# Kernel optimization log

Measured on AMD Instinct MI355X. Metric: run time of the kernel, lower is better.

Reference implementation:

```python
import jax, jax.numpy as jnp
import numpy as np

EPS = 1e-5

def conv2d(x, w, pad):
    # x: NCHW, w: OIHW
    return jax.lax.conv_general_dilated(
        x, w, window_strides=(1, 1), padding=[(pad, pad), (pad, pad)],
        dimension_numbers=("NCHW", "OIHW", "NCHW"))

def instnorm(x, gamma=None, beta=None):
    # per-(N,C) normalization over H,W (biased variance, like torch InstanceNorm2d)
    mu = jnp.mean(x, axis=(2, 3), keepdims=True)
    var = jnp.mean((x - mu) ** 2, axis=(2, 3), keepdims=True)
    y = (x - mu) * jax.lax.rsqrt(var + EPS)
    if gamma is not None:
        y = y * gamma[None, :, None, None] + beta[None, :, None, None]
    return y

def ode_rhs(y, W, b):
    # conv -> relu -> instance norm (no affine) -> conv_transpose(same weight) -> -1 (stable)
    z = conv2d(y, W, 1) + b[None, :, None, None]
    z = jax.nn.relu(z)
    z = instnorm(z)
    # ConvTranspose2d with weight W (in,out,kh,kw here square C,C) == conv with
    # channel-swapped, spatially flipped kernel, SAME padding.
    Wt = jnp.transpose(jnp.flip(W, axis=(2, 3)), (1, 0, 2, 3))
    z = conv2d(z, Wt, 1)
    return -z

def ode_block(y, Wbank, bbank):
    # RK4 over t_grid = linspace(0,1,5): 4 steps of dt = 0.25.
    # Piecewise-constant weights: floor(t*4) clamped -> stages 1-3 of step i use
    # bank[i]; stage 4 (at t_{i+1}) uses bank[min(i+1, 3)].
    n = Wbank.shape[0]
    dt = 1.0 / n
    for i in range(n):
        j = min(i + 1, n - 1)
        k1 = ode_rhs(y, Wbank[i], bbank[i])
        k2 = ode_rhs(y + 0.5 * dt * k1, Wbank[i], bbank[i])
        k3 = ode_rhs(y + 0.5 * dt * k2, Wbank[i], bbank[i])
        k4 = ode_rhs(y + dt * k3, Wbank[j], bbank[j])
        y = y + (dt / 6.0) * (k1 + 2.0 * k2 + 2.0 * k3 + k4)
    return y

def avgpool2(x):
    N, C, H, W = x.shape
    return x.reshape(N, C, H // 2, 2, W // 2, 2).mean(axis=(3, 5))

def forward(x, stem_w, stem_b, norm1_g, norm1_b, ode1_W, ode1_b,
            conn1_w, conn1_b, norm3_g, norm3_b, ode2_W, ode2_b,
            conn2_w, conn2_b, norm4_g, norm4_b, ode3_W, ode3_b,
            head_w, head_b):
    x = conv2d(x, stem_w, 1) + stem_b[None, :, None, None]
    x = instnorm(x, norm1_g, norm1_b)
    x = jax.nn.relu(x)
    x = ode_block(x, ode1_W, ode1_b)
    x = conv2d(x, conn1_w, 0) + conn1_b[None, :, None, None]
    x = instnorm(x, norm3_g, norm3_b)
    x = jax.nn.relu(x)
    x = avgpool2(x)
    x = ode_block(x, ode2_W, ode2_b)
    x = conv2d(x, conn2_w, 0) + conn2_b[None, :, None, None]
    x = instnorm(x, norm4_g, norm4_b)
    x = jax.nn.relu(x)
    x = avgpool2(x)
    x = ode_block(x, ode3_W, ode3_b)
    x = x.mean(axis=(2, 3))  # AdaptiveAvgPool2d(1) + Flatten -> [N, 4*ch]
    return x @ head_w.T + head_b

def setup_inputs() -> dict:
    key = jax.random.key(0)
    ks = jax.random.split(key, 16)
    ch = 64
    f = jnp.float32
    d = {
        "x": jax.random.normal(ks[0], (8, 3, 96, 96), f),
        "stem_w": jax.random.normal(ks[1], (ch, 3, 3, 3), f) * 0.1,
        "stem_b": jnp.zeros((ch,), f),
        "norm1_g": jnp.ones((ch,), f),
        "norm1_b": jnp.zeros((ch,), f),
        "ode1_W": jax.random.normal(ks[2], (4, ch, ch, 3, 3), f) * 0.1,
        "ode1_b": jnp.zeros((4, ch), f),
        "conn1_w": jax.random.normal(ks[3], (2 * ch, ch, 1, 1), f) * 0.1,
        "conn1_b": jnp.zeros((2 * ch,), f),
        "norm3_g": jnp.ones((2 * ch,), f),
        "norm3_b": jnp.zeros((2 * ch,), f),
        "ode2_W": jax.random.normal(ks[4], (4, 2 * ch, 2 * ch, 3, 3), f) * 0.1,
        "ode2_b": jnp.zeros((4, 2 * ch), f),
        "conn2_w": jax.random.normal(ks[5], (4 * ch, 2 * ch, 1, 1), f) * 0.1,
        "conn2_b": jnp.zeros((4 * ch,), f),
        "norm4_g": jnp.ones((4 * ch,), f),
        "norm4_b": jnp.zeros((4 * ch,), f),
        "ode3_W": jax.random.normal(ks[6], (4, 4 * ch, 4 * ch, 3, 3), f) * 0.1,
        "ode3_b": jnp.zeros((4, 4 * ch), f),
        "head_w": jax.random.normal(ks[7], (10, 4 * ch), f) * 0.05,
        "head_b": jnp.zeros((10,), f),
    }
    return d

def reference(x, stem_w, stem_b, norm1_g, norm1_b, ode1_W, ode1_b,
              conn1_w, conn1_b, norm3_g, norm3_b, ode2_W, ode2_b,
              conn2_w, conn2_b, norm4_g, norm4_b, ode3_W, ode3_b,
              head_w, head_b):
    return forward(x, stem_w, stem_b, norm1_g, norm1_b, ode1_W, ode1_b,
                   conn1_w, conn1_b, norm3_g, norm3_b, ode2_W, ode2_b,
                   conn2_w, conn2_b, norm4_g, norm4_b, ode3_W, ode3_b,
                   head_w, head_b)
```

## Files before the change

### kernel.cpp

```cpp
#include <hip/hip_runtime.h>


typedef __attribute__((ext_vector_type(8)))  short  s16x8;
typedef __attribute__((ext_vector_type(16))) float  f32x16;

__device__ __forceinline__ unsigned short bf16_rtne(float f) {
    unsigned u = __builtin_bit_cast(unsigned, f);
    unsigned r = u + 0x7FFFu + ((u >> 16) & 1u);
    return (unsigned short)(r >> 16);
}
__device__ __forceinline__ void split2(float v, unsigned& h, unsigned& l) {
    unsigned u = __builtin_bit_cast(unsigned, v);
    h = (u + 0x7fffu + ((u >> 16) & 1u)) >> 16;
    float r = v - __builtin_bit_cast(float, h << 16);
    unsigned ur = __builtin_bit_cast(unsigned, r);
    l = (ur + 0x7fffu + ((ur >> 16) & 1u)) >> 16;
}
__device__ __forceinline__ unsigned packsplit(float v) {
    unsigned h, l; split2(v, h, l); return h | (l << 16);
}

__global__ __launch_bounds__(256) void pack_weights(
    const float* __restrict__ Wb, unsigned short* __restrict__ out, int C)
{
    const int dir = blockIdx.y;
    const int MT = C >> 5, ICC = C >> 4;
    const size_t TOT = (size_t)36 * C * C;
    size_t t = (size_t)blockIdx.x * 256 + threadIdx.x;
    if (t >= TOT) return;
    int j = t & 7;
    int l = (t >> 3) & 63;
    size_t r = t >> 9;
    int kp  = r % 9;  r /= 9;
    int mt  = r % MT; r /= MT;
    int icc = r % ICC; r /= ICC;
    int bank = (int)r;
    int oc = mt * 32 + (l & 31);
    int ic = icc * 16 + (l >> 5) * 8 + j;
    int kh = kp / 3, kw = kp % 3;
    float v;
    if (dir == 0)
        v = Wb[(((size_t)(bank * C + oc) * C + ic) * 3 + kh) * 3 + kw];
    else
        v = Wb[(((size_t)(bank * C + ic) * C + oc) * 3 + (2 - kh)) * 3 + (2 - kw)];
    unsigned short h = bf16_rtne(v);
    float hf = __builtin_bit_cast(float, (unsigned)h << 16);
    unsigned short lo = bf16_rtne(v - hf);
    size_t idx = ((((size_t)bank * ICC + icc) * MT + mt) * 9 + kp) * 1024 + l * 8 + j;
    unsigned short* base = out + (size_t)dir * 72 * C * C;
    base[idx] = h;
    base[idx + 512] = lo;
}

template<int NW, int MODE>
__global__ __launch_bounds__(NW * 64) void conv_mfma4(
    const void* __restrict__ in,
    const unsigned short* __restrict__ pA,
    const float* __restrict__ bias,
    const float* __restrict__ partI,
    float* __restrict__ partO,
    const float* __restrict__ ybase, float* __restrict__ accb,
    float* __restrict__ ydstF, unsigned* __restrict__ ydstS,
    int C, int H, int W, int tilesX, int tilesT, float inv_hw,
    int mode, float acoef, float dt6)
{
    constexpr bool CONV2 = (MODE == 2);
    constexpr int TPX = 16, TPY = 2 * NW;
    constexpr int HX = TPX + 2, HY = TPY + 2;
    constexpr int NROW = HX * HY;
    constexpr int RS = 20;
    constexpr int PL = NROW * RS;
    constexpr int BUFS = 2 * PL;
    constexpr int NTHR = NW * 64;
    constexpr int NELEM = NROW * 16;
    constexpr int NIT = (NELEM + NTHR - 1) / NTHR;
    __shared__ __align__(16) unsigned short sB[2 * BUFS];
    __shared__ float sTab[CONV2 ? 512 : 4];

    const int tid = threadIdx.x;
    const int w = tid >> 6, lane = tid & 63;
    const int n = blockIdx.x;
    const int tile = blockIdx.y;
    const int mt = blockIdx.z;
    const int tileX = tile % tilesX, tileY = tile / tilesX;
    const int px0 = tileX * TPX, py0 = tileY * TPY;
    const int ocb = mt * 32;
    const int HW = H * W;
    const int ICC = C >> 4, MT = C >> 5;
    const int col = lane & 31, half = lane >> 5;
    const int xl = col & 15, yr = col >> 4;
    const int wy0 = 2 * w;
    const int ncbase = n * C;

    float stg[NIT];
    auto stageLoad = [&](int icc) {
#pragma unroll
        for (int i = 0; i < NIT; i++) {
            int e = tid + i * NTHR;
            float v = 0.f;
            if (e < NELEM) {
                int ic = e / NROW; int r = e - ic * NROW;
                int yy = r / HX, xx = r - yy * HX;
                int gy = py0 + yy - 1, gx = px0 + xx - 1;
                if (gy >= 0 && gy < H && gx >= 0 && gx < W) {
                    int c = icc * 16 + ic;
                    size_t ad = (size_t)(ncbase + c) * HW + gy * W + gx;
                    if (MODE == 0)
                        v = ((const float*)in)[ad];
                    else
                        v = __builtin_bit_cast(float, ((const unsigned*)in)[ad]);
                }
            }
            stg[i] = v;
        }
    };
    auto stageWrite = [&](int b, int c0) {
#pragma unroll
        for (int i = 0; i < NIT; i++) {
            int e = tid + i * NTHR;
            if (e < NELEM) {
                int ic = e / NROW; int r = e - ic * NROW;
                unsigned h, l;
                if (MODE == 1) {
                    unsigned u = __builtin_bit_cast(unsigned, stg[i]);
                    h = u & 0xffffu; l = u >> 16;
                } else if (MODE == 2) {
                    int yy = r / HX, xx = r - yy * HX;
                    int gy = py0 + yy - 1, gx = px0 + xx - 1;
                    float v = 0.f;
                    if (gy >= 0 && gy < H && gx >= 0 && gx < W) {
                        unsigned u = __builtin_bit_cast(unsigned, stg[i]);
                        float vh = __builtin_bit_cast(float, u << 16);
                        float vl = __builtin_bit_cast(float, u & 0xffff0000u);
                        int c = c0 + ic;
                        v = (vh + vl - sTab[2 * c]) * sTab[2 * c + 1];
                    }
                    split2(v, h, l);
                } else {
                    split2(stg[i], h, l);
                }
                int off = b * BUFS + r * RS + ic;
                sB[off] = (unsigned short)h;
                sB[off + PL] = (unsigned short)l;
            }
        }
    };
    auto loadB = [&](int b, int kp, s16x8& oh, s16x8& ol) {
        int kh = kp / 3, kw = kp - kh * 3;
        int px = (wy0 + yr + kh) * HX + (xl + kw);
        int off = b * BUFS + px * RS + half * 8;
        oh = *(const s16x8*)&sB[off];
        ol = *(const s16x8*)&sB[off + PL];
    };

    f32x16 accA{}, accB{}, accC{};

    stageLoad(0);

    if (CONV2) {
        for (int c0 = tid; c0 < C; c0 += NTHR) {
            int mtc = c0 >> 5, occ = c0 & 31;
            const float* pb = partI + ((size_t)(n * MT + mtc) * tilesT) * 64 + occ;
            float s = 0.f, q = 0.f;
#pragma unroll 4
            for (int tt = 0; tt < tilesT; ++tt) {
                s += pb[(size_t)tt * 64];
                q += pb[(size_t)tt * 64 + 32];
            }
            float m = s * inv_hw;
            sTab[2 * c0] = m;
            sTab[2 * c0 + 1] = rsqrtf(fmaf(-m, m, q * inv_hw) + 1e-5f);
        }
        __syncthreads();
    }

    stageWrite(0, 0);
    __syncthreads();

    for (int icc = 0; icc < ICC; ++icc) {
        s16x8 aH[9], aL[9];
        {
            const unsigned short* ab =
                pA + ((size_t)(icc * MT + mt)) * 9216 + lane * 8;
#pragma unroll
            for (int kp = 0; kp < 9; ++kp) {
                aH[kp] = *(const s16x8*)(ab + kp * 1024);
                aL[kp] = *(const s16x8*)(ab + kp * 1024 + 512);
            }
        }
        const int b = icc & 1;
        if (icc + 1 < ICC) stageLoad(icc + 1);

        s16x8 bh, bl;
        loadB(b, 0, bh, bl);
#pragma unroll
        for (int kp = 0; kp < 9; ++kp) {
            s16x8 bhn, bln;
            if (kp < 8) loadB(b, kp + 1, bhn, bln);
            accA = __builtin_amdgcn_mfma_f32_32x32x16_bf16(aH[kp], bh, accA, 0, 0, 0);
            accB = __builtin_amdgcn_mfma_f32_32x32x16_bf16(aL[kp], bh, accB, 0, 0, 0);
            accC = __builtin_amdgcn_mfma_f32_32x32x16_bf16(aH[kp], bl, accC, 0, 0, 0);
            if (kp < 8) { bh = bhn; bl = bln; }
        }
        if (icc + 1 < ICC) {
            stageWrite(b ^ 1, (icc + 1) * 16);
            __syncthreads();
        }
    }

    const int gx = px0 + xl;
    const int gy = py0 + wy0 + yr;
    const bool valid = (gx < W);
    float* sred = (float*)sB;
#pragma unroll
    for (int r = 0; r < 16; r++) {
        int row = (r & 3) + 8 * (r >> 2) + 4 * half;
        int oc = ocb + row;
        size_t idx = (size_t)(ncbase + oc) * HW + (size_t)gy * W + gx;
        float v = accA[r] + accB[r] + accC[r];
        if (!CONV2) {
            v += bias[oc];
            v = fmaxf(v, 0.f);
            if (valid) ydstS[idx] = packsplit(v);
            float s = valid ? v : 0.f;
            float sq = s * s;
#pragma unroll
            for (int m = 1; m < 32; m <<= 1) {
                s  += __shfl_xor(s, m, 64);
                sq += __shfl_xor(sq, m, 64);
            }
            if ((lane & 31) == 0) {
                int slot = ((w * 2 + half) * 16 + r) * 2;
                sred[slot] = s;
                sred[slot + 1] = sq;
            }
        } else if (valid) {
            float k = -v;
            if (mode == 0) {
                accb[idx] = k;
                ydstS[idx] = packsplit(ybase[idx] + acoef * k);
            } else if (mode == 3) {
                ydstF[idx] = ybase[idx] + dt6 * (accb[idx] + k);
            } else {
                accb[idx] += 2.f * k;
                ydstS[idx] = packsplit(ybase[idx] + acoef * k);
            }
        }
    }
    if (!CONV2) {
        __syncthreads();
        if (tid < 32) {
            int h2 = (tid >> 2) & 1;
            int r  = (tid & 3) | ((tid >> 3) << 2);
            float s = 0.f, sq = 0.f;
#pragma unroll
            for (int wv = 0; wv < NW; wv++) {
                int slot = ((wv * 2 + h2) * 16 + r) * 2;
                s  += sred[slot];
                sq += sred[slot + 1];
            }
            float* po = partO + ((size_t)(n * MT + mt) * tilesT + tile) * 64;
            po[tid] = s;
            po[tid + 32] = sq;
        }
    }
}

__global__ __launch_bounds__(256) void conv3x3_stem(
    const float* __restrict__ in, const float* __restrict__ w,
    const float* __restrict__ bias, float* __restrict__ out,
    int H, int W, int tilesX)
{
    __shared__ float sIn[3][18][34];
    __shared__ float sW[16][3][9];
    const int tid = threadIdx.x;
    const int tx = tid & 15, ty = tid >> 4;
    const int tileX = blockIdx.x % tilesX, tileY = blockIdx.x / tilesX;
    const int x0 = tileX * 32, y0 = tileY * 16;
    const int oc0 = blockIdx.y * 16;
    const int n = blockIdx.z;
    const int HW = H * W;

    for (int idx = tid; idx < 3 * 18 * 34; idx += 256) {
        int c = idx / (18 * 34); int r = idx % (18 * 34);
        int iy = r / 34, ix = r % 34;
        int gy = y0 + iy - 1, gx = x0 + ix - 1;
        float v = 0.f;
        if (gy >= 0 && gy < H && gx >= 0 && gx < W)
            v = in[(size_t)(n * 3 + c) * HW + gy * W + gx];
        sIn[c][iy][ix] = v;
    }
    for (int idx = tid; idx < 16 * 27; idx += 256) {
        int o = idx / 27, r = idx % 27;
        sW[o][r / 9][r % 9] = w[(size_t)(oc0 + o) * 27 + r];
    }
    __syncthreads();

    float a0[16], a1[16];
#pragma unroll
    for (int o = 0; o < 16; o++) { a0[o] = 0.f; a1[o] = 0.f; }
#pragma unroll
    for (int c = 0; c < 3; c++)
#pragma unroll
        for (int kh = 0; kh < 3; kh++)
#pragma unroll
            for (int kw = 0; kw < 3; kw++) {
                float v0 = sIn[c][ty + kh][tx + kw];
                float v1 = sIn[c][ty + kh][tx + 16 + kw];
#pragma unroll
                for (int o = 0; o < 16; o++) {
                    float wv = sW[o][c][kh * 3 + kw];
                    a0[o] = fmaf(v0, wv, a0[o]);
                    a1[o] = fmaf(v1, wv, a1[o]);
                }
            }

    const int gy = y0 + ty, gx = x0 + tx;
#pragma unroll
    for (int o = 0; o < 16; o++) {
        float bb = bias[oc0 + o];
        size_t base = (size_t)(n * 64 + oc0 + o) * HW + (size_t)gy * W + gx;
        out[base] = a0[o] + bb;
        out[base + 16] = a1[o] + bb;
    }
}

__global__ __launch_bounds__(256) void stats_kernel(
    const float* __restrict__ x, float* __restrict__ mu, float* __restrict__ rstd,
    int HW, float inv_hw)
{
    int nc = blockIdx.x;
    const float* p = x + (size_t)nc * HW;
    float s = 0.f, ss = 0.f;
    for (int i = threadIdx.x; i < HW; i += 256) {
        float v = p[i];
        s += v;
        ss = fmaf(v, v, ss);
    }
    for (int off = 32; off; off >>= 1) {
        s  += __shfl_down(s, off, 64);
        ss += __shfl_down(ss, off, 64);
    }
    __shared__ float aS[4], aSS[4];
    int wid = threadIdx.x >> 6, lane = threadIdx.x & 63;
    if (lane == 0) { aS[wid] = s; aSS[wid] = ss; }
    __syncthreads();
    if (threadIdx.x == 0) {
        s  = aS[0] + aS[1] + aS[2] + aS[3];
        ss = aSS[0] + aSS[1] + aSS[2] + aSS[3];
        float m = s * inv_hw;
        float var = fmaf(-m, m, ss * inv_hw);
        mu[nc] = m;
        rstd[nc] = rsqrtf(var + 1e-5f);
    }
}

__global__ __launch_bounds__(256) void norm_affine_relu_kernel(
    const float* __restrict__ in, float* __restrict__ out,
    const float* __restrict__ mu, const float* __restrict__ rstd,
    const float* __restrict__ g, const float* __restrict__ b,
    int C, int HW, size_t total)
{
    size_t i = (size_t)blockIdx.x * 256 + threadIdx.x;
    if (i >= total) return;
    size_t nc = i / HW;
    int c = (int)(nc % C);
    float v = (in[i] - mu[nc]) * rstd[nc] * g[c] + b[c];
    out[i] = fmaxf(v, 0.f);
}

__global__ __launch_bounds__(256) void norm_pool_kernel(
    const float* __restrict__ in, float* __restrict__ out,
    const float* __restrict__ mu, const float* __restrict__ rstd,
    const float* __restrict__ g, const float* __restrict__ b,
    int C, int Ho, int Wo, size_t total)
{
    size_t i = (size_t)blockIdx.x * 256 + threadIdx.x;
    if (i >= total) return;
    int wo = (int)(i % Wo);
    int ho = (int)((i / Wo) % Ho);
    size_t nc = i / ((size_t)Wo * Ho);
    int c = (int)(nc % C);
    const int Wi = 2 * Wo;
    const float* p = in + nc * (size_t)(4 * Ho * Wo) + (size_t)(2 * ho) * Wi + 2 * wo;
    float sc  = rstd[nc] * g[c];
    float off = fmaf(-mu[nc], sc, b[c]);
    float2 t0 = *(const float2*)p;
    float2 t1 = *(const float2*)(p + Wi);
    float s = fmaxf(fmaf(t0.x, sc, off), 0.f) + fmaxf(fmaf(t0.y, sc, off), 0.f)
            + fmaxf(fmaf(t1.x, sc, off), 0.f) + fmaxf(fmaf(t1.y, sc, off), 0.f);
    out[i] = 0.25f * s;
}

#define C1OCT 8
__global__ __launch_bounds__(256) void conv1x1_kernel(
    const float* __restrict__ in, const float* __restrict__ w,
    const float* __restrict__ bias, float* __restrict__ out,
    int Cin, int Cout, int HW)
{
    const int HW4 = HW >> 2;
    int p = blockIdx.x * 256 + threadIdx.x;
    if (p >= HW4) return;
    const int oc0 = blockIdx.y * C1OCT;
    const int n = blockIdx.z;
    const float4* ip = (const float4*)(in + (size_t)n * Cin * HW) + p;
    float acc[C1OCT][4];
#pragma unroll
    for (int o = 0; o < C1OCT; o++)
        acc[o][0] = acc[o][1] = acc[o][2] = acc[o][3] = 0.f;
#pragma unroll 4
    for (int ic = 0; ic < Cin; ic++) {
        float4 v = ip[(size_t)ic * HW4];
#pragma unroll
        for (int o = 0; o < C1OCT; o++) {
            float wv = w[(size_t)(oc0 + o) * Cin + ic];
            acc[o][0] = fmaf(v.x, wv, acc[o][0]);
            acc[o][1] = fmaf(v.y, wv, acc[o][1]);
            acc[o][2] = fmaf(v.z, wv, acc[o][2]);
            acc[o][3] = fmaf(v.w, wv, acc[o][3]);
        }
    }
    float4* op = (float4*)(out + ((size_t)n * Cout + oc0) * HW) + p;
#pragma unroll
    for (int o = 0; o < C1OCT; o++) {
        float bb = bias[oc0 + o];
        float4 r;
        r.x = acc[o][0] + bb; r.y = acc[o][1] + bb;
        r.z = acc[o][2] + bb; r.w = acc[o][3] + bb;
        op[(size_t)o * HW4] = r;
    }
}

__global__ __launch_bounds__(128) void head_kernel(
    const float* __restrict__ m, const float* __restrict__ hw,
    const float* __restrict__ hb, float* __restrict__ out, int C)
{
    int t = threadIdx.x;
    if (t < 80) {
        int n = t / 10, k = t % 10;
        float acc = hb[k];
        for (int c = 0; c < C; c++)
            acc = fmaf(m[n * C + c], hw[k * C + c], acc);
        out[t] = acc;
    }
}

struct OdeCfg { int C, H, tilesX, tilesT; };
static const OdeCfg CFG[3] = {
    {64, 96, 6, 36},
    {128, 48, 3, 18},
    {256, 24, 2, 6},
};

static void launch_c1(int st, int inMode, const void* in, const unsigned short* pA,
                      const float* bias, float* part, unsigned* z, hipStream_t s)
{
    const OdeCfg& c = CFG[st];
    dim3 g(8, c.tilesT, c.C / 32);
    float ih = 1.f / (c.H * c.H);
    if (st == 0) {
        if (inMode == 0)
            conv_mfma4<8, 0><<<g, 512, 0, s>>>(in, pA, bias,
                nullptr, part, nullptr, nullptr, nullptr, z,
                c.C, c.H, c.H, c.tilesX, c.tilesT, ih, 0, 0.f, 0.f);
        else
            conv_mfma4<8, 1><<<g, 512, 0, s>>>(in, pA, bias,
                nullptr, part, nullptr, nullptr, nullptr, z,
                c.C, c.H, c.H, c.tilesX, c.tilesT, ih, 0, 0.f, 0.f);
    } else {
        if (inMode == 0)
            conv_mfma4<4, 0><<<g, 256, 0, s>>>(in, pA, bias,
                nullptr, part, nullptr, nullptr, nullptr, z,
                c.C, c.H, c.H, c.tilesX, c.tilesT, ih, 0, 0.f, 0.f);
        else
            conv_mfma4<4, 1><<<g, 256, 0, s>>>(in, pA, bias,
                nullptr, part, nullptr, nullptr, nullptr, z,
                c.C, c.H, c.H, c.tilesX, c.tilesT, ih, 0, 0.f, 0.f);
    }
}

static void launch_c2(int st, const unsigned* z, const unsigned short* pA,
                      const float* part,
                      const float* ybase, float* accb,
                      float* ydstF, unsigned* ydstS,
                      int mode, float acoef, hipStream_t s)
{
    const OdeCfg& c = CFG[st];
    dim3 g(8, c.tilesT, c.C / 32);
    float ih = 1.f / (c.H * c.H);
    const float dt6 = 0.25f / 6.f;
    if (st == 0)
        conv_mfma4<8, 2><<<g, 512, 0, s>>>(z, pA, nullptr,
            part, nullptr, ybase, accb, ydstF, ydstS,
            c.C, c.H, c.H, c.tilesX, c.tilesT, ih, mode, acoef, dt6);
    else
        conv_mfma4<4, 2><<<g, 256, 0, s>>>(z, pA, nullptr,
            part, nullptr, ybase, accb, ydstF, ydstS,
            c.C, c.H, c.H, c.tilesX, c.tilesT, ih, mode, acoef, dt6);
}

static void ode_block_mfma(int st, float* y, unsigned* t, unsigned* z, float* a,
                           float* part, unsigned short* pack,
                           const float* bbank, hipStream_t s)
{
    const OdeCfg& c = CFG[st];
    const int C = c.C;
    const size_t BANKW = (size_t)18 * C * C;
    const size_t DIRW  = (size_t)72 * C * C;
    const float dt = 0.25f;
    for (int i = 0; i < 4; i++) {
        int j = (i + 1 > 3) ? 3 : i + 1;
        const unsigned short* p1  = pack + i * BANKW;
        const unsigned short* p1t = pack + DIRW + i * BANKW;
        const unsigned short* p4  = pack + j * BANKW;
        const unsigned short* p4t = pack + DIRW + j * BANKW;
        const float* b1 = bbank + (size_t)i * C;
        const float* b4 = bbank + (size_t)j * C;

        launch_c1(st, 0, y, p1, b1, part, z, s);
        launch_c2(st, z, p1t, part, y, a, nullptr, t, 0, 0.5f * dt, s);
        launch_c1(st, 1, t, p1, b1, part, z, s);
        launch_c2(st, z, p1t, part, y, a, nullptr, t, 1, 0.5f * dt, s);
        launch_c1(st, 1, t, p1, b1, part, z, s);
        launch_c2(st, z, p1t, part, y, a, nullptr, t, 1, dt, s);
        launch_c1(st, 1, t, p4, b4, part, z, s);
        launch_c2(st, z, p4t, part, y, a, y, t, 3, 0.f, s);
    }
}

extern "C" void kernel_launch(void* const* d_in, const int* in_sizes, int n_in,
                              void* d_out, int out_size, void* d_ws, size_t ws_size,
                              hipStream_t stream)
{
    const float* x       = (const float*)d_in[0];
    const float* stem_w  = (const float*)d_in[1];
    const float* stem_b  = (const float*)d_in[2];
    const float* norm1_g = (const float*)d_in[3];
    const float* norm1_b = (const float*)d_in[4];
    const float* ode1_W  = (const float*)d_in[5];
    const float* ode1_b  = (const float*)d_in[6];
    const float* conn1_w = (const float*)d_in[7];
    const float* conn1_b = (const float*)d_in[8];
    const float* norm3_g = (const float*)d_in[9];
    const float* norm3_b = (const float*)d_in[10];
    const float* ode2_W  = (const float*)d_in[11];
    const float* ode2_b  = (const float*)d_in[12];
    const float* conn2_w = (const float*)d_in[13];
    const float* conn2_b = (const float*)d_in[14];
    const float* norm4_g = (const float*)d_in[15];
    const float* norm4_b = (const float*)d_in[16];
    const float* ode3_W  = (const float*)d_in[17];
    const float* ode3_b  = (const float*)d_in[18];
    const float* head_w  = (const float*)d_in[19];
    const float* head_b  = (const float*)d_in[20];
    float* out = (float*)d_out;

    float* ws = (float*)d_ws;
    const size_t BUF = 4718592;
    float*    y  = ws;
    unsigned* t  = (unsigned*)(ws + BUF);
    unsigned* z  = (unsigned*)(ws + 2 * BUF);
    float*    a  = ws + 3 * BUF;
    float*    mu = ws + 4 * BUF;
    float*    rs = mu + 2048;
    float*    part = ws + 4 * BUF + 4096;
    unsigned short* pack = (unsigned short*)(ws + 4 * BUF + 4096 + 36864);
    float* tf = (float*)t;

    {
        int H = 96;
        dim3 grid(3 * 6, 4, 8);
        conv3x3_stem<<<grid, 256, 0, stream>>>(x, stem_w, stem_b, (float*)z,
                                               H, H, 3);
        stats_kernel<<<8 * 64, 256, 0, stream>>>((float*)z, mu, rs, H * H, 1.f / (H * H));
        size_t total = (size_t)8 * 64 * H * H;
        norm_affine_relu_kernel<<<(total + 255) / 256, 256, 0, stream>>>(
            (float*)z, y, mu, rs, norm1_g, norm1_b, 64, H * H, total);
    }

    {
        size_t TOT = (size_t)36 * 64 * 64;
        pack_weights<<<dim3((TOT + 255) / 256, 2), 256, 0, stream>>>(ode1_W, pack, 64);
        ode_block_mfma(0, y, t, z, a, part, pack, ode1_b, stream);
    }

    {
        int H = 96, HW = H * H, Cin = 64, Cout = 128;
        dim3 grid((HW / 4 + 255) / 256, Cout / C1OCT, 8);
        conv1x1_kernel<<<grid, 256, 0, stream>>>(y, conn1_w, conn1_b, tf, Cin, Cout, HW);
        stats_kernel<<<8 * Cout, 256, 0, stream>>>(tf, mu, rs, HW, 1.f / HW);
        size_t ptotal = (size_t)8 * Cout * 48 * 48;
        norm_pool_kernel<<<(ptotal + 255) / 256, 256, 0, stream>>>(
            tf, y, mu, rs, norm3_g, norm3_b, Cout, 48, 48, ptotal);
    }

    {
        size_t TOT = (size_t)36 * 128 * 128;
        pack_weights<<<dim3((TOT + 255) / 256, 2), 256, 0, stream>>>(ode2_W, pack, 128);
        ode_block_mfma(1, y, t, z, a, part, pack, ode2_b, stream);
    }

    {
        int H = 48, HW = H * H, Cin = 128, Cout = 256;
        dim3 grid((HW / 4 + 255) / 256, Cout / C1OCT, 8);
        conv1x1_kernel<<<grid, 256, 0, stream>>>(y, conn2_w, conn2_b, tf, Cin, Cout, HW);
        stats_kernel<<<8 * Cout, 256, 0, stream>>>(tf, mu, rs, HW, 1.f / HW);
        size_t ptotal = (size_t)8 * Cout * 24 * 24;
        norm_pool_kernel<<<(ptotal + 255) / 256, 256, 0, stream>>>(
            tf, y, mu, rs, norm4_g, norm4_b, Cout, 24, 24, ptotal);
    }

    {
        size_t TOT = (size_t)36 * 256 * 256;
        pack_weights<<<dim3((TOT + 255) / 256, 2), 256, 0, stream>>>(ode3_W, pack, 256);
        ode_block_mfma(2, y, t, z, a, part, pack, ode3_b, stream);
    }

    {
        int H = 24, HW = H * H, C = 256;
        stats_kernel<<<8 * C, 256, 0, stream>>>(y, mu, rs, HW, 1.f / HW);
        head_kernel<<<1, 128, 0, stream>>>(mu, head_w, head_b, out, C);
    }
}
```

Before: 5.394 ms.

## Use 4-wave conv blocks for stage 0, add occupancy hints and parallel stats reduction

```diff
diff --git a/kernel.cpp b/kernel.cpp
--- a/kernel.cpp
+++ b/kernel.cpp
@@ -53,7 +53,7 @@
 }
 
 template<int NW, int MODE>
-__global__ __launch_bounds__(NW * 64) void conv_mfma4(
+__global__ __launch_bounds__(NW * 64, NW == 4 ? 5 : 2) void conv_mfma4(
     const void* __restrict__ in,
     const unsigned short* __restrict__ pA,
     const float* __restrict__ bias,
@@ -158,18 +158,31 @@
     stageLoad(0);
 
     if (CONV2) {
-        for (int c0 = tid; c0 < C; c0 += NTHR) {
+        float* sRed = (float*)sB;
+        const int g = NTHR / C;
+        {
+            int c0 = tid % C, sl = tid / C;
             int mtc = c0 >> 5, occ = c0 & 31;
+            int t0 = (tilesT * sl) / g, t1 = (tilesT * (sl + 1)) / g;
             const float* pb = partI + ((size_t)(n * MT + mtc) * tilesT) * 64 + occ;
+            float S = 0.f, Q = 0.f;
+            for (int tt = t0; tt < t1; ++tt) {
+                S += pb[(size_t)tt * 64];
+                Q += pb[(size_t)tt * 64 + 32];
+            }
+            sRed[tid] = S;
+            sRed[NTHR + tid] = Q;
+        }
+        __syncthreads();
+        if (tid < C) {
             float s = 0.f, q = 0.f;
-#pragma unroll 4
-            for (int tt = 0; tt < tilesT; ++tt) {
-                s += pb[(size_t)tt * 64];
-                q += pb[(size_t)tt * 64 + 32];
+            for (int k = 0; k < g; ++k) {
+                s += sRed[k * C + tid];
+                q += sRed[NTHR + k * C + tid];
             }
             float m = s * inv_hw;
-            sTab[2 * c0] = m;
-            sTab[2 * c0 + 1] = rsqrtf(fmaf(-m, m, q * inv_hw) + 1e-5f);
+            sTab[2 * tid] = m;
+            sTab[2 * tid + 1] = rsqrtf(fmaf(-m, m, q * inv_hw) + 1e-5f);
         }
         __syncthreads();
     }
@@ -447,7 +460,7 @@
 
 struct OdeCfg { int C, H, tilesX, tilesT; };
 static const OdeCfg CFG[3] = {
-    {64, 96, 6, 36},
+    {64, 96, 6, 72},
     {128, 48, 3, 18},
     {256, 24, 2, 6},
 };
@@ -458,25 +471,14 @@
     const OdeCfg& c = CFG[st];
     dim3 g(8, c.tilesT, c.C / 32);
     float ih = 1.f / (c.H * c.H);
-    if (st == 0) {
-        if (inMode == 0)
-            conv_mfma4<8, 0><<<g, 512, 0, s>>>(in, pA, bias,
-                nullptr, part, nullptr, nullptr, nullptr, z,
-                c.C, c.H, c.H, c.tilesX, c.tilesT, ih, 0, 0.f, 0.f);
-        else
-            conv_mfma4<8, 1><<<g, 512, 0, s>>>(in, pA, bias,
-                nullptr, part, nullptr, nullptr, nullptr, z,
-                c.C, c.H, c.H, c.tilesX, c.tilesT, ih, 0, 0.f, 0.f);
-    } else {
-        if (inMode == 0)
-            conv_mfma4<4, 0><<<g, 256, 0, s>>>(in, pA, bias,
-                nullptr, part, nullptr, nullptr, nullptr, z,
-                c.C, c.H, c.H, c.tilesX, c.tilesT, ih, 0, 0.f, 0.f);
-        else
-            conv_mfma4<4, 1><<<g, 256, 0, s>>>(in, pA, bias,
-                nullptr, part, nullptr, nullptr, nullptr, z,
-                c.C, c.H, c.H, c.tilesX, c.tilesT, ih, 0, 0.f, 0.f);
-    }
+    if (inMode == 0)
+        conv_mfma4<4, 0><<<g, 256, 0, s>>>(in, pA, bias,
+            nullptr, part, nullptr, nullptr, nullptr, z,
+            c.C, c.H, c.H, c.tilesX, c.tilesT, ih, 0, 0.f, 0.f);
+    else
+        conv_mfma4<4, 1><<<g, 256, 0, s>>>(in, pA, bias,
+            nullptr, part, nullptr, nullptr, nullptr, z,
+            c.C, c.H, c.H, c.tilesX, c.tilesT, ih, 0, 0.f, 0.f);
 }
 
 static void launch_c2(int st, const unsigned* z, const unsigned short* pA,
@@ -489,14 +491,9 @@
     dim3 g(8, c.tilesT, c.C / 32);
     float ih = 1.f / (c.H * c.H);
     const float dt6 = 0.25f / 6.f;
-    if (st == 0)
-        conv_mfma4<8, 2><<<g, 512, 0, s>>>(z, pA, nullptr,
-            part, nullptr, ybase, accb, ydstF, ydstS,
-            c.C, c.H, c.H, c.tilesX, c.tilesT, ih, mode, acoef, dt6);
-    else
-        conv_mfma4<4, 2><<<g, 256, 0, s>>>(z, pA, nullptr,
-            part, nullptr, ybase, accb, ydstF, ydstS,
-            c.C, c.H, c.H, c.tilesX, c.tilesT, ih, mode, acoef, dt6);
+    conv_mfma4<4, 2><<<g, 256, 0, s>>>(z, pA, nullptr,
+        part, nullptr, ybase, accb, ydstF, ydstS,
+        c.C, c.H, c.H, c.tilesX, c.tilesT, ih, mode, acoef, dt6);
 }
 
 static void ode_block_mfma(int st, float* y, unsigned* t, unsigned* z, float* a,
@@ -564,7 +561,7 @@
     float*    mu = ws + 4 * BUF;
     float*    rs = mu + 2048;
     float*    part = ws + 4 * BUF + 4096;
-    unsigned short* pack = (unsigned short*)(ws + 4 * BUF + 4096 + 36864);
+    unsigned short* pack = (unsigned short*)(ws + 4 * BUF + 4096 + 73728);
     float* tf = (float*)t;
 
     {
```

New measurement: 20.89 ms. 287% more time.
